# Optimization experiments

Hardware: AMD Instinct MI355X
Metric: run time of the kernel (lower is better)

## Reference

```python
import jax, jax.numpy as jnp
import numpy as np

N_GRAPHS = 1250
NEG_SLOPE = 0.2

def gat_layer(x, src, dst, W, a_src, a_dst, b, concat):
    # x: [N, Fin]; W: [Fin, H*C]; a_src/a_dst: [H, C]; b: [H*C] or [C]
    N = x.shape[0]
    H, C = a_src.shape
    h = (x @ W).reshape(N, H, C)                      # [N,H,C]
    alpha_s = jnp.sum(h * a_src[None], axis=-1)       # [N,H]
    alpha_d = jnp.sum(h * a_dst[None], axis=-1)       # [N,H]
    e = jax.nn.leaky_relu(alpha_s[src] + alpha_d[dst], NEG_SLOPE)  # [E,H]
    # segment softmax over incoming edges of each target node
    m = jax.ops.segment_max(e, dst, num_segments=N)   # [N,H]
    m = jnp.where(jnp.isfinite(m), m, 0.0)
    ex = jnp.exp(e - m[dst])
    s = jax.ops.segment_sum(ex, dst, num_segments=N)  # [N,H]
    alpha = ex / (s[dst] + 1e-16)                     # [E,H]
    msg = h[src] * alpha[..., None]                   # [E,H,C]
    out = jax.ops.segment_sum(msg, dst, num_segments=N)  # [N,H,C]
    out = out.reshape(N, H * C) if concat else out.mean(axis=1)
    return out + b

def setup_inputs() -> dict:
    key = jax.random.key(0)
    ks = jax.random.split(key, 13)
    N, E = 50000, 100000
    x = jax.random.normal(ks[0], (N, 78), dtype=jnp.float32)
    edge_index = jax.random.randint(ks[1], (2, E), 0, N, dtype=jnp.int64)
    # sorted segment ids -> every graph non-empty (~40 nodes each)
    batch = jnp.sort(jax.random.randint(ks[2], (N,), 0, N_GRAPHS, dtype=jnp.int64))
    g = lambda k, shape, fan: jax.random.normal(k, shape, dtype=jnp.float32) / np.float32(np.sqrt(fan))
    return {
        'x': x, 'edge_index': edge_index, 'batch': batch,
        'W1': g(ks[3], (78, 780), 78), 'a_src1': g(ks[4], (10, 78), 78), 'a_dst1': g(ks[5], (10, 78), 78),
        'b1': jnp.zeros((780,), jnp.float32),
        'W2': g(ks[6], (780, 128), 780), 'a_src2': g(ks[7], (1, 128), 128), 'a_dst2': g(ks[8], (1, 128), 128),
        'b2': jnp.zeros((128,), jnp.float32),
        'fc_w': g(ks[9], (128, 128), 128), 'fc_b': jnp.zeros((128,), jnp.float32),
    }

def reference(x, edge_index, batch, W1, a_src1, a_dst1, b1, W2, a_src2, a_dst2, b2, fc_w, fc_b):
    N = x.shape[0]
    loop = jnp.arange(N, dtype=edge_index.dtype)
    src = jnp.concatenate([edge_index[0], loop])  # add self loops (PyG default)
    dst = jnp.concatenate([edge_index[1], loop])
    # dropout layers are identity in eval mode
    h = jax.nn.elu(gat_layer(x, src, dst, W1, a_src1, a_dst1, b1, concat=True))   # [N,780]
    h = jax.nn.relu(gat_layer(h, src, dst, W2, a_src2, a_dst2, b2, concat=True))  # [N,128]
    g = jax.ops.segment_max(h, batch, num_segments=N_GRAPHS)                      # [G,128]
    g = jnp.where(jnp.isfinite(g), g, 0.0)
    return jax.nn.relu(g @ fc_w + fc_b)
```

## Files before the change

### kernel.cpp

```cpp
#include <hip/hip_runtime.h>
#include <hip/hip_bf16.h>
#include <cstdint>

#define CAP 32
typedef __hip_bfloat16 bf16;
typedef __attribute__((ext_vector_type(8))) short short8;
typedef __attribute__((ext_vector_type(4))) float f32x4;

__device__ __forceinline__ float sb2f(short s) {
  unsigned int u = ((unsigned int)(unsigned short)s) << 16;
  return __uint_as_float(u);
}
__device__ __forceinline__ short f2sb(float f) {
  bf16 h = __float2bfloat16(f);
  return *reinterpret_cast<short*>(&h);
}

__global__ void k_detect(const int* __restrict__ ei, int* __restrict__ flag) {
  __shared__ int any;
  if (threadIdx.x == 0) any = 0;
  __syncthreads();
  int v = 0;
  for (int i = 1 + 2 * threadIdx.x; i < 2000; i += 512) v |= ei[i];
  if (v) atomicOr(&any, 1);
  __syncthreads();
  if (threadIdx.x == 0) flag[0] = (any == 0) ? 1 : 0;
}

__device__ __forceinline__ void edge_sd(const int* __restrict__ ei, int e, int f,
                                        int& src, int& dst) {
  if (e < 100000) {
    if (f) { src = ei[2 * e]; dst = ei[200000 + 2 * e]; }
    else   { src = ei[e];     dst = ei[100000 + e]; }
  } else { src = dst = e - 100000; }
  src = min(max(src, 0), 49999);
  dst = min(max(dst, 0), 49999);
}

__global__ void k_prep(const float* __restrict__ x, const float* __restrict__ W1,
                       const float* __restrict__ W2, const float* __restrict__ aw1,
                       const float* __restrict__ dw1, bf16* __restrict__ xb,
                       bf16* __restrict__ W1t, bf16* __restrict__ W2t,
                       bf16* __restrict__ Wat, float* __restrict__ zp, int zeroWords) {
  int i = blockIdx.x * 256 + threadIdx.x;
  if (i < zeroWords) zp[i] = 0.f;
  const int n_xb = 50000 * 96;
  const int n_w1 = 832 * 96;
  const int n_w2 = 128 * 832;
  const int n_wa = 32 * 96;
  if (i < n_xb) {
    int r = i / 96, k = i - r * 96;
    xb[i] = __float2bfloat16(k < 78 ? x[r * 78 + k] : 0.f);
  } else if (i < n_xb + n_w1) {
    int j = i - n_xb;
    int n = j / 96, k = j - n * 96;
    W1t[j] = __float2bfloat16((k < 78 && n < 780) ? W1[k * 780 + n] : 0.f);
  } else if (i < n_xb + n_w1 + n_w2) {
    int j = i - n_xb - n_w1;
    int c = j / 832, k = j - c * 832;
    W2t[j] = __float2bfloat16(k < 780 ? W2[k * 128 + c] : 0.f);
  } else if (i < n_xb + n_w1 + n_w2 + n_wa) {
    int j = i - n_xb - n_w1 - n_w2;
    int c = j / 96, k = j - c * 96;
    float s = 0.f;
    if (k < 78 && c < 20) {
      const float* w = (c < 10) ? aw1 : dw1;
      int h = (c < 10) ? c : c - 10;
      const float* wrow = W1 + k * 780 + h * 78;
      const float* arow = w + h * 78;
      for (int q = 0; q < 78; q++) s += wrow[q] * arow[q];
    }
    Wat[c * 96 + k] = __float2bfloat16(s);
  }
}

__global__ __launch_bounds__(256) void k_gemm1(const bf16* __restrict__ xb,
                                               const bf16* __restrict__ W1t,
                                               const bf16* __restrict__ Wat,
                                               const float* __restrict__ b1,
                                               bf16* __restrict__ H1,
                                               float* __restrict__ as1,
                                               float* __restrict__ ad1) {
  __shared__ __align__(16) short Als[64 * 104];
  __shared__ __align__(16) short Bls[64 * 104];
  __shared__ __align__(16) short Wls[32 * 104];
  __shared__ __align__(16) float Cls[64 * 68];
  __shared__ float b1s[832];
  const int t = threadIdx.x;
  const int w = t >> 6, l = t & 63, l15 = l & 15, q = l >> 4;
  const int rowBase = blockIdx.x * 64;
  for (int s = t; s < 768; s += 256) {
    int row = s / 12, kg = s - row * 12;
    short8 v = {};
    int gr = rowBase + row;
    if (gr < 50000) v = *(const short8*)((const short*)xb + (size_t)gr * 96 + kg * 8);
    *(short8*)&Als[row * 104 + kg * 8] = v;
  }
  for (int s = t; s < 384; s += 256) {
    int row = s / 12, kg = s - row * 12;
    *(short8*)&Wls[row * 104 + kg * 8] =
        *(const short8*)((const short*)Wat + (size_t)row * 96 + kg * 8);
  }
  for (int s = t; s < 832; s += 256) b1s[s] = (s < 780) ? b1[s] : 0.f;
  short8 breg[3];
  int bn[3], bk[3];
#pragma unroll
  for (int i = 0; i < 3; i++) {
    int s = t + i * 256;
    bn[i] = s / 12; bk[i] = s - bn[i] * 12;
    breg[i] = *(const short8*)((const short*)W1t + (size_t)bn[i] * 96 + bk[i] * 8);
  }
  for (int cc = 0; cc < 13; cc++) {
    __syncthreads();
#pragma unroll
    for (int i = 0; i < 3; i++) *(short8*)&Bls[bn[i] * 104 + bk[i] * 8] = breg[i];
    if (cc < 12) {
#pragma unroll
      for (int i = 0; i < 3; i++)
        breg[i] = *(const short8*)((const short*)W1t +
                                   (size_t)((cc + 1) * 64 + bn[i]) * 96 + bk[i] * 8);
    }
    __syncthreads();
    f32x4 acc[4] = {};
#pragma unroll
    for (int ks = 0; ks < 3; ks++) {
      short8 a = *(const short8*)&Als[(w * 16 + l15) * 104 + ks * 32 + q * 8];
#pragma unroll
      for (int nt = 0; nt < 4; nt++) {
        short8 b = *(const short8*)&Bls[(nt * 16 + l15) * 104 + ks * 32 + q * 8];
        acc[nt] = __builtin_amdgcn_mfma_f32_16x16x32_bf16(a, b, acc[nt], 0, 0, 0);
      }
    }
    __syncthreads();
#pragma unroll
    for (int nt = 0; nt < 4; nt++)
#pragma unroll
      for (int r = 0; r < 4; r++)
        Cls[(w * 16 + q * 4 + r) * 68 + nt * 16 + l15] = acc[nt][r];
    __syncthreads();
    {
      int r = t >> 2, c0 = (t & 3) * 16;
      int gr = rowBase + r;
      if (gr < 50000) {
        short8 o0, o1;
#pragma unroll
        for (int c = 0; c < 8; c++) o0[c] = f2sb(Cls[r * 68 + c0 + c] + b1s[cc * 64 + c0 + c]);
#pragma unroll
        for (int c = 0; c < 8; c++) o1[c] = f2sb(Cls[r * 68 + c0 + 8 + c] + b1s[cc * 64 + c0 + 8 + c]);
        short* dst = (short*)H1 + (size_t)gr * 832 + cc * 64 + c0;
        *(short8*)dst = o0;
        *(short8*)(dst + 8) = o1;
      }
    }
  }
  f32x4 acc2[2] = {};
#pragma unroll
  for (int ks = 0; ks < 3; ks++) {
    short8 a = *(const short8*)&Als[(w * 16 + l15) * 104 + ks * 32 + q * 8];
#pragma unroll
    for (int nt = 0; nt < 2; nt++) {
      short8 b = *(const short8*)&Wls[(nt * 16 + l15) * 104 + ks * 32 + q * 8];
      acc2[nt] = __builtin_amdgcn_mfma_f32_16x16x32_bf16(a, b, acc2[nt], 0, 0, 0);
    }
  }
  const int gr0 = rowBase + w * 16 + q * 4;
#pragma unroll
  for (int nt = 0; nt < 2; nt++) {
    int c = nt * 16 + l15;
#pragma unroll
    for (int r = 0; r < 4; r++) {
      int gr = gr0 + r;
      if (gr < 50000) {
        if (c < 10)       as1[gr * 10 + c] = acc2[nt][r];
        else if (c < 20)  ad1[gr * 10 + (c - 10)] = acc2[nt][r];
      }
    }
  }
}

__global__ void k_scatter(const int* __restrict__ ei, const int* __restrict__ flag,
                          int* __restrict__ cnt, int* __restrict__ csr) {
  int e = blockIdx.x * 256 + threadIdx.x;
  if (e >= 150000) return;
  int f = flag[0], src, dst;
  edge_sd(ei, e, f, src, dst);
  int pos = atomicAdd(&cnt[dst], 1);
  if (pos < CAP) csr[dst * CAP + pos] = src;
}

__global__ __launch_bounds__(128) void k_agg1(const bf16* __restrict__ H1,
                                              const float* __restrict__ as1,
                                              const float* __restrict__ ad1,
                                              const int* __restrict__ csr,
                                              const int* __restrict__ cnt,
                                              bf16* __restrict__ HL2) {
  __shared__ float sexw[CAP * 10];
  __shared__ float sden[16];
  __shared__ float sad[10];
  __shared__ int ssrc[CAP];
  __shared__ int scnt;
  const int t = threadIdx.x;
  const int n = blockIdx.x;
  if (t == 0) scnt = min(cnt[n], CAP);
  if (t >= 16 && t < 32) sden[t - 16] = 0.f;
  if (t >= 32 && t < 42) sad[t - 32] = ad1[n * 10 + (t - 32)];
  __syncthreads();
  const int cn = scnt;
  if (t < cn) {
    int src = csr[n * CAP + t];
    ssrc[t] = src;
    const float2* ap = (const float2*)(as1 + src * 10);
    float av[10];
#pragma unroll
    for (int i = 0; i < 5; i++) { float2 qq = ap[i]; av[2 * i] = qq.x; av[2 * i + 1] = qq.y; }
#pragma unroll
    for (int h = 0; h < 10; h++) {
      float e = av[h] + sad[h];
      e = e >= 0.f ? e : 0.2f * e;
      float ex = __expf(e);
      sexw[t * 10 + h] = ex;
      atomicAdd(&sden[h], ex);
    }
  }
  __syncthreads();
  if (t < 104) {
    const int j0 = t * 8;
    const int h0u = j0 / 78;
    const int hsplit = (h0u + 1) * 78 - j0;
    const int h1u = (j0 + 7) / 78;
    const int h0 = min(h0u, 9), h1 = min(h1u, 9);
    const float* sw = sexw;
    const short* base = (const short*)H1 + j0;
    float acc[8] = {};
    if (cn > 0) {
      short8 v0 = *(const short8*)(base + (size_t)ssrc[0] * 832);
      short8 v1 = v0;
      if (cn > 1) v1 = *(const short8*)(base + (size_t)ssrc[1] * 832);
      int k = 0;
      for (; k + 2 < cn; k += 2) {
        short8 p0 = *(const short8*)(base + (size_t)ssrc[k + 2] * 832);
        short8 p1 = p0;
        if (k + 3 < cn) p1 = *(const short8*)(base + (size_t)ssrc[k + 3] * 832);
        {
          float w0 = sw[k * 10 + h0], w1 = sw[k * 10 + h1];
#pragma unroll
          for (int c = 0; c < 8; c++) acc[c] += (c < hsplit ? w0 : w1) * sb2f(v0[c]);
          float u0 = sw[(k + 1) * 10 + h0], u1 = sw[(k + 1) * 10 + h1];
#pragma unroll
          for (int c = 0; c < 8; c++) acc[c] += (c < hsplit ? u0 : u1) * sb2f(v1[c]);
        }
        v0 = p0; v1 = p1;
      }
      {
        float w0 = sw[k * 10 + h0], w1 = sw[k * 10 + h1];
#pragma unroll
        for (int c = 0; c < 8; c++) acc[c] += (c < hsplit ? w0 : w1) * sb2f(v0[c]);
      }
      if (k + 1 < cn) {
        float u0 = sw[(k + 1) * 10 + h0], u1 = sw[(k + 1) * 10 + h1];
#pragma unroll
        for (int c = 0; c < 8; c++) acc[c] += (c < hsplit ? u0 : u1) * sb2f(v1[c]);
      }
    }
    const float r0 = 1.f / (sden[h0] + 1e-16f);
    const float r1 = 1.f / (sden[h1] + 1e-16f);
    short8 ov;
#pragma unroll
    for (int c = 0; c < 8; c++) {
      float v = acc[c] * (c < hsplit ? r0 : r1);
      v = v > 0.f ? v : __expf(v) - 1.f;
      ov[c] = f2sb(v);
    }
    *(short8*)((short*)HL2 + (size_t)n * 832 + j0) = ov;
  }
}

__global__ __launch_bounds__(256) void k_gemm2(const bf16* __restrict__ A,
                                               const bf16* __restrict__ W2t,
                                               const float* __restrict__ AW2,
                                               const float* __restrict__ DW2,
                                               bf16* __restrict__ H2,
                                               float* __restrict__ as2,
                                               float* __restrict__ ad2) {
  __shared__ __align__(16) short Als[64 * 72];
  __shared__ __align__(16) short Bls[128 * 72];
  __shared__ float sAW[128], sDW[128];
  __shared__ float sS[4][64], sD[4][64];
  const int t = threadIdx.x;
  const int w = t >> 6, l = t & 63, l15 = l & 15, q = l >> 4;
  const int rowBase = blockIdx.x * 64;
  if (t < 128) sAW[t] = AW2[t];
  else         sDW[t - 128] = DW2[t - 128];
  const int ar = t >> 2, ak = t & 3;
  short8 areg[2], breg[4];
  {
    int gr0 = rowBase + ar;
#pragma unroll
    for (int i = 0; i < 2; i++) {
      short8 v = {};
      int gr = gr0;
      if (gr < 50000)
        v = *(const short8*)((const short*)A + (size_t)gr * 832 + 0 + (ak * 2 + i) * 8);
      areg[i] = v;
    }
#pragma unroll
    for (int i = 0; i < 4; i++) {
      int s = t + i * 256;
      int col = s >> 3, kg = s & 7;
      breg[i] = *(const short8*)((const short*)W2t + (size_t)col * 832 + 0 + kg * 8);
    }
  }
  f32x4 acc[4][2] = {};
  for (int kb = 0; kb < 832; kb += 64) {
    __syncthreads();
#pragma unroll
    for (int i = 0; i < 2; i++)
      *(short8*)&Als[ar * 72 + (ak * 2 + i) * 8] = areg[i];
#pragma unroll
    for (int i = 0; i < 4; i++) {
      int s = t + i * 256;
      int col = s >> 3, kg = s & 7;
      *(short8*)&Bls[col * 72 + kg * 8] = breg[i];
    }
    if (kb < 768) {
      int kn = kb + 64;
      int gr = rowBase + ar;
#pragma unroll
      for (int i = 0; i < 2; i++) {
        short8 v = {};
        if (gr < 50000)
          v = *(const short8*)((const short*)A + (size_t)gr * 832 + kn + (ak * 2 + i) * 8);
        areg[i] = v;
      }
#pragma unroll
      for (int i = 0; i < 4; i++) {
        int s = t + i * 256;
        int col = s >> 3, kg = s & 7;
        breg[i] = *(const short8*)((const short*)W2t + (size_t)col * 832 + kn + kg * 8);
      }
    }
    __syncthreads();
#pragma unroll
    for (int ks = 0; ks < 2; ks++) {
      short8 a[4];
#pragma unroll
      for (int mt = 0; mt < 4; mt++)
        a[mt] = *(const short8*)&Als[(mt * 16 + l15) * 72 + ks * 32 + q * 8];
#pragma unroll
      for (int ntl = 0; ntl < 2; ntl++) {
        short8 b = *(const short8*)&Bls[((w * 2 + ntl) * 16 + l15) * 72 + ks * 32 + q * 8];
#pragma unroll
        for (int mt = 0; mt < 4; mt++)
          acc[mt][ntl] = __builtin_amdgcn_mfma_f32_16x16x32_bf16(a[mt], b, acc[mt][ntl], 0, 0, 0);
      }
    }
  }
  const int col0 = w * 32 + l15, col1 = col0 + 16;
  const float aw0 = sAW[col0], aw1 = sAW[col1];
  const float dw0 = sDW[col0], dw1 = sDW[col1];
  f32x4 sp[4], dp[4];
#pragma unroll
  for (int mt = 0; mt < 4; mt++) {
    sp[mt] = acc[mt][0] * aw0 + acc[mt][1] * aw1;
    dp[mt] = acc[mt][0] * dw0 + acc[mt][1] * dw1;
  }
#pragma unroll
  for (int m = 1; m < 16; m <<= 1) {
#pragma unroll
    for (int mt = 0; mt < 4; mt++)
#pragma unroll
      for (int r = 0; r < 4; r++) {
        sp[mt][r] += __shfl_xor(sp[mt][r], m, 64);
        dp[mt][r] += __shfl_xor(dp[mt][r], m, 64);
      }
  }
  if (l15 == 0) {
#pragma unroll
    for (int mt = 0; mt < 4; mt++)
#pragma unroll
      for (int r = 0; r < 4; r++) {
        sS[w][mt * 16 + q * 4 + r] = sp[mt][r];
        sD[w][mt * 16 + q * 4 + r] = dp[mt][r];
      }
  }
#pragma unroll
  for (int mt = 0; mt < 4; mt++) {
    int gr0 = rowBase + mt * 16 + q * 4;
#pragma unroll
    for (int ntl = 0; ntl < 2; ntl++) {
      int gc = w * 32 + ntl * 16 + l15;
#pragma unroll
      for (int r = 0; r < 4; r++) {
        int gr = gr0 + r;
        if (gr < 50000) H2[(size_t)gr * 128 + gc] = __float2bfloat16(acc[mt][ntl][r]);
      }
    }
  }
  __syncthreads();
  if (t < 64) {
    int gr = rowBase + t;
    if (gr < 50000) as2[gr] = sS[0][t] + sS[1][t] + sS[2][t] + sS[3][t];
  } else if (t < 128) {
    int r2 = t - 64;
    int gr = rowBase + r2;
    if (gr < 50000) ad2[gr] = sD[0][r2] + sD[1][r2] + sD[2][r2] + sD[3][r2];
  }
}

__global__ __launch_bounds__(128) void k_agg2(const bf16* __restrict__ H2,
                                              const float* __restrict__ as2,
                                              const float* __restrict__ ad2,
                                              const int* __restrict__ csr,
                                              const int* __restrict__ cnt,
                                              const float* __restrict__ b2,
                                              const int* __restrict__ batch,
                                              const int* __restrict__ flag,
                                              float* __restrict__ g) {
  __shared__ int ssrc[CAP];
  __shared__ float sexw[CAP];
  __shared__ float sden;
  __shared__ int scnt, sbv;
  const int t = threadIdx.x;
  const int n = blockIdx.x;
  if (t == 0) {
    scnt = min(cnt[n], CAP);
    sden = 0.f;
    int b = flag[0] ? batch[2 * n] : batch[n];
    sbv = min(max(b, 0), 1249);
  }
  __syncthreads();
  const int cn = scnt;
  if (t < cn) {
    int src = csr[n * CAP + t];
    ssrc[t] = src;
    float e = as2[src] + ad2[n];
    e = e >= 0.f ? e : 0.2f * e;
    float ex = __expf(e);
    sexw[t] = ex;
    atomicAdd(&sden, ex);
  }
  __syncthreads();
  const short* H2s = (const short*)H2;
  float acc = 0.f;
  if (cn > 0) {
    short hv = H2s[(size_t)ssrc[0] * 128 + t];
    for (int k = 0; k < cn; k++) {
      short hn = hv;
      if (k + 1 < cn) hn = H2s[(size_t)ssrc[k + 1] * 128 + t];
      acc += sexw[k] * sb2f(hv);
      hv = hn;
    }
  }
  float v = acc / (sden + 1e-16f) + b2[t];
  v = v > 0.f ? v : 0.f;
  atomicMax((int*)&g[sbv * 128 + t], __float_as_int(v));
}

__global__ __launch_bounds__(128) void k_fc(const float* __restrict__ g,
                                            const float* __restrict__ fw,
                                            const float* __restrict__ fb,
                                            float* __restrict__ out) {
  const int n = blockIdx.x, t = threadIdx.x;
  __shared__ float grow[128];
  grow[t] = g[n * 128 + t];
  __syncthreads();
  float acc = fb[t];
  for (int k = 0; k < 128; k++) acc += grow[k] * fw[k * 128 + t];
  out[n * 128 + t] = acc > 0.f ? acc : 0.f;
}

extern "C" void kernel_launch(void* const* d_in, const int* in_sizes, int n_in,
                              void* d_out, int out_size, void* d_ws, size_t ws_size,
                              hipStream_t stream) {
  const float* x     = (const float*)d_in[0];
  const int*   ei    = (const int*)d_in[1];
  const int*   batch = (const int*)d_in[2];
  const float* W1    = (const float*)d_in[3];
  const float* as1w  = (const float*)d_in[4];
  const float* ad1w  = (const float*)d_in[5];
  const float* b1    = (const float*)d_in[6];
  const float* W2    = (const float*)d_in[7];
  const float* as2w  = (const float*)d_in[8];
  const float* ad2w  = (const float*)d_in[9];
  const float* b2    = (const float*)d_in[10];
  const float* fcw   = (const float*)d_in[11];
  const float* fcb   = (const float*)d_in[12];
  float* out = (float*)d_out;

  char* p = (char*)d_ws;
  size_t off = 0;
  auto alloc = [&](size_t bytes) -> void* {
    void* r = p + off;
    off = (off + bytes + 15) & ~(size_t)15;
    return r;
  };
  int*   cnt = (int*)  alloc(50000 * 4);
  float* g   = (float*)alloc(160000 * 4);
  size_t zeroWords = off / 4;
  float* as1 = (float*)alloc(500000 * 4);
  float* ad1 = (float*)alloc(500000 * 4);
  float* as2 = (float*)alloc(50000 * 4);
  float* ad2 = (float*)alloc(50000 * 4);
  bf16*  W1t = (bf16*) alloc((size_t)832 * 96 * 2);
  bf16*  W2t = (bf16*) alloc((size_t)128 * 832 * 2);
  bf16*  Wat = (bf16*) alloc((size_t)32 * 96 * 2);
  bf16*  h1  = (bf16*) alloc((size_t)50000 * 832 * 2);
  bf16*  hl2 = (bf16*) alloc((size_t)50000 * 832 * 2);
  int*   csr = (int*)  alloc((size_t)50000 * CAP * 4);
  void*  uni = alloc((size_t)50000 * 128 * 2);
  bf16*  xb  = (bf16*)uni;
  bf16*  h2  = (bf16*)uni;
  int*   flag = (int*) alloc(16);
  (void)ws_size; (void)in_sizes; (void)n_in; (void)out_size;

  k_detect<<<1, 256, 0, stream>>>(ei, flag);
  int prepN = 50000 * 96 + 832 * 96 + 128 * 832 + 32 * 96;
  k_prep<<<(prepN + 255) / 256, 256, 0, stream>>>(
      x, W1, W2, as1w, ad1w, xb, W1t, W2t, Wat, (float*)d_ws, (int)zeroWords);

  k_gemm1<<<782, 256, 0, stream>>>(xb, W1t, Wat, b1, h1, as1, ad1);
  k_scatter<<<(150000 + 255) / 256, 256, 0, stream>>>(ei, flag, cnt, csr);
  k_agg1<<<50000, 128, 0, stream>>>(h1, as1, ad1, csr, cnt, hl2);
  k_gemm2<<<782, 256, 0, stream>>>(hl2, W2t, as2w, ad2w, h2, as2, ad2);
  k_agg2<<<50000, 128, 0, stream>>>(h2, as2, ad2, csr, cnt, b2, batch, flag, g);
  k_fc<<<1250, 128, 0, stream>>>(g, fcw, fcb, out);
}
```

Baseline: 310.0 us.

## Stage neighbor rows in LDS cooperatively, processing two nodes per block in agg1

Reworks the layer-1 aggregation so each 256-thread block handles two destination nodes. All threads cooperatively load the neighbor feature rows into shared memory in chunks of 16, overlapping the gathers with the attention-weight computation, and then accumulate from LDS. This replaces the per-thread serial global gathers, which used only 104 of 128 threads, with wider, more parallel loads. The cost is about 26KB of LDS per block, which lowers occupancy, plus extra block-wide syncs.

```diff
diff --git a/kernel.cpp b/kernel.cpp
--- a/kernel.cpp
+++ b/kernel.cpp
@@ -3,6 +3,7 @@
 #include <cstdint>
 
 #define CAP 32
+#define SMAX 16
 typedef __hip_bfloat16 bf16;
 typedef __attribute__((ext_vector_type(8))) short short8;
 typedef __attribute__((ext_vector_type(4))) float f32x4;
@@ -188,82 +189,87 @@
   if (pos < CAP) csr[dst * CAP + pos] = src;
 }
 
-__global__ __launch_bounds__(128) void k_agg1(const bf16* __restrict__ H1,
+__global__ __launch_bounds__(256) void k_agg1(const bf16* __restrict__ H1,
                                               const float* __restrict__ as1,
                                               const float* __restrict__ ad1,
                                               const int* __restrict__ csr,
                                               const int* __restrict__ cnt,
                                               bf16* __restrict__ HL2) {
-  __shared__ float sexw[CAP * 10];
-  __shared__ float sden[16];
-  __shared__ float sad[10];
-  __shared__ int ssrc[CAP];
-  __shared__ int scnt;
+  __shared__ __align__(16) short Hst[SMAX * 832];
+  __shared__ float sexw[2][CAP * 10];
+  __shared__ float sden[2][16];
+  __shared__ int ssrc[2][CAP];
+  __shared__ int scnt[2];
   const int t = threadIdx.x;
-  const int n = blockIdx.x;
-  if (t == 0) scnt = min(cnt[n], CAP);
-  if (t >= 16 && t < 32) sden[t - 16] = 0.f;
-  if (t >= 32 && t < 42) sad[t - 32] = ad1[n * 10 + (t - 32)];
-  __syncthreads();
-  const int cn = scnt;
-  if (t < cn) {
-    int src = csr[n * CAP + t];
-    ssrc[t] = src;
-    const float2* ap = (const float2*)(as1 + src * 10);
-    float av[10];
-#pragma unroll
-    for (int i = 0; i < 5; i++) { float2 qq = ap[i]; av[2 * i] = qq.x; av[2 * i + 1] = qq.y; }
-#pragma unroll
-    for (int h = 0; h < 10; h++) {
-      float e = av[h] + sad[h];
-      e = e >= 0.f ? e : 0.2f * e;
-      float ex = __expf(e);
-      sexw[t * 10 + h] = ex;
-      atomicAdd(&sden[h], ex);
-    }
-  }
-  __syncthreads();
-  if (t < 104) {
-    const int j0 = t * 8;
-    const int h0u = j0 / 78;
-    const int hsplit = (h0u + 1) * 78 - j0;
-    const int h1u = (j0 + 7) / 78;
-    const int h0 = min(h0u, 9), h1 = min(h1u, 9);
-    const float* sw = sexw;
-    const short* base = (const short*)H1 + j0;
-    float acc[8] = {};
-    if (cn > 0) {
-      short8 v0 = *(const short8*)(base + (size_t)ssrc[0] * 832);
-      short8 v1 = v0;
-      if (cn > 1) v1 = *(const short8*)(base + (size_t)ssrc[1] * 832);
-      int k = 0;
-      for (; k + 2 < cn; k += 2) {
-        short8 p0 = *(const short8*)(base + (size_t)ssrc[k + 2] * 832);
-        short8 p1 = p0;
-        if (k + 3 < cn) p1 = *(const short8*)(base + (size_t)ssrc[k + 3] * 832);
-        {
-          float w0 = sw[k * 10 + h0], w1 = sw[k * 10 + h1];
-#pragma unroll
-          for (int c = 0; c < 8; c++) acc[c] += (c < hsplit ? w0 : w1) * sb2f(v0[c]);
-          float u0 = sw[(k + 1) * 10 + h0], u1 = sw[(k + 1) * 10 + h1];
-#pragma unroll
-          for (int c = 0; c < 8; c++) acc[c] += (c < hsplit ? u0 : u1) * sb2f(v1[c]);
-        }
-        v0 = p0; v1 = p1;
-      }
-      {
-        float w0 = sw[k * 10 + h0], w1 = sw[k * 10 + h1];
-#pragma unroll
-        for (int c = 0; c < 8; c++) acc[c] += (c < hsplit ? w0 : w1) * sb2f(v0[c]);
-      }
-      if (k + 1 < cn) {
-        float u0 = sw[(k + 1) * 10 + h0], u1 = sw[(k + 1) * 10 + h1];
-#pragma unroll
-        for (int c = 0; c < 8; c++) acc[c] += (c < hsplit ? u0 : u1) * sb2f(v1[c]);
-      }
-    }
-    const float r0 = 1.f / (sden[h0] + 1e-16f);
-    const float r1 = 1.f / (sden[h1] + 1e-16f);
+  const int sub = t >> 7, tt = t & 127;
+  const int n = blockIdx.x * 2 + sub;
+  if (t < 2) scnt[t] = min(cnt[blockIdx.x * 2 + t], CAP);
+  if (t >= 32 && t < 64) { int z = t - 32; sden[z >> 4][z & 15] = 0.f; }
+  __syncthreads();
+  const int cn = scnt[sub];
+  const int cn0 = scnt[0];
+  const int K_tot = scnt[0] + scnt[1];
+  if (tt < cn) ssrc[sub][tt] = csr[n * CAP + tt];
+  __syncthreads();
+
+  const int j0 = tt * 8;
+  int hj[8];
+#pragma unroll
+  for (int c = 0; c < 8; c++) { int h = (j0 + c) / 78; hj[c] = h > 9 ? 9 : h; }
+  float acc[8] = {};
+  const short* H1s = (const short*)H1;
+
+  for (int c0 = 0; c0 < K_tot; c0 += SMAX) {
+    const int nsl = min(SMAX, K_tot - c0);
+    const int nch = nsl * 104;
+    short8 st[7];
+#pragma unroll
+    for (int i = 0; i < 7; i++) {
+      int ci = t + i * 256;
+      if (ci < nch) {
+        int s = c0 + ci / 104, col = ci - (ci / 104) * 104;
+        int sb = (s >= cn0) ? 1 : 0;
+        int idx = s - (sb ? cn0 : 0);
+        int srow = ssrc[sb][idx];
+        st[i] = *(const short8*)(H1s + (size_t)srow * 832 + col * 8);
+      }
+    }
+    if (c0 == 0) {
+      for (int wv = tt; wv < cn * 10; wv += 128) {
+        int k = wv / 10, h = wv - k * 10;
+        int src = ssrc[sub][k];
+        float e = as1[src * 10 + h] + ad1[n * 10 + h];
+        e = e >= 0.f ? e : 0.2f * e;
+        float ex = __expf(e);
+        sexw[sub][wv] = ex;
+        atomicAdd(&sden[sub][h], ex);
+      }
+    }
+#pragma unroll
+    for (int i = 0; i < 7; i++) {
+      int ci = t + i * 256;
+      if (ci < nch) *(short8*)&Hst[ci * 8] = st[i];
+    }
+    __syncthreads();
+    if (tt < 104) {
+      int k_lo = sub ? max(0, c0 - cn0) : c0;
+      int k_hi = sub ? min(K_tot - cn0, c0 + nsl - cn0) : min(cn0, c0 + nsl);
+      int rbase = (sub ? cn0 : 0) - c0;
+      const float* sw = sexw[sub];
+      for (int k = k_lo; k < k_hi; k++) {
+        short8 hv = *(const short8*)&Hst[(rbase + k) * 832 + j0];
+        const float* swk = sw + k * 10;
+#pragma unroll
+        for (int c = 0; c < 8; c++) acc[c] += swk[hj[c]] * sb2f(hv[c]);
+      }
+    }
+    if (c0 + SMAX < K_tot) __syncthreads();
+  }
+  if (tt < 104) {
+    const int h0 = hj[0], h1 = hj[7];
+    const int hsplit = (j0 / 78 + 1) * 78 - j0;
+    const float r0 = 1.f / (sden[sub][h0] + 1e-16f);
+    const float r1 = 1.f / (sden[sub][h1] + 1e-16f);
     short8 ov;
 #pragma unroll
     for (int c = 0; c < 8; c++) {
@@ -520,7 +526,7 @@
 
   k_gemm1<<<782, 256, 0, stream>>>(xb, W1t, Wat, b1, h1, as1, ad1);
   k_scatter<<<(150000 + 255) / 256, 256, 0, stream>>>(ei, flag, cnt, csr);
-  k_agg1<<<50000, 128, 0, stream>>>(h1, as1, ad1, csr, cnt, hl2);
+  k_agg1<<<25000, 256, 0, stream>>>(h1, as1, ad1, csr, cnt, hl2);
   k_gemm2<<<782, 256, 0, stream>>>(hl2, W2t, as2w, ad2w, h2, as2, ad2);
   k_agg2<<<50000, 128, 0, stream>>>(h2, as2, ad2, csr, cnt, b2, batch, flag, g);
   k_fc<<<1250, 128, 0, stream>>>(g, fcw, fcb, out);
```

After: 334.3 us. 1.08x slower.
